# Kernel tuning notes

Hardware: AMD Instinct MI355X
Metric: run time of the kernel (lower is better)

## Reference

```python
import jax, jax.numpy as jnp
import numpy as np

N, E, G, H = 4096, 8192, 64, 128  # nodes, edges, graphs, hidden dim
NODE_DIM, EDGE_DIM = 11, 5


def _linear_params(key, fan_in, fan_out):
    kw, kb = jax.random.split(key)
    s = 1.0 / np.sqrt(fan_in)
    w = jax.random.uniform(kw, (fan_in, fan_out), minval=-s, maxval=s, dtype=jnp.float32)
    b = jax.random.uniform(kb, (fan_out,), minval=-s, maxval=s, dtype=jnp.float32)
    return w, b


def setup_inputs() -> dict:
    key = jax.random.key(0)
    ks = jax.random.split(key, 10)
    x = jax.random.normal(ks[0], (N, NODE_DIM), dtype=jnp.float32)
    edge_attr = jax.random.normal(ks[1], (E, EDGE_DIM), dtype=jnp.float32)
    edge_index = jax.random.randint(ks[2], (2, E), 0, N, dtype=jnp.int64)
    batch = jnp.sort(jax.random.randint(ks[3], (N,), 0, G, dtype=jnp.int64))
    # preprocess MLP: node_dim -> 128 -> 128
    p1_w, p1_b = _linear_params(ks[4], NODE_DIM, H)
    p2_w, p2_b = _linear_params(ks[5], H, H)
    # edge net: edge_dim -> 128 -> 256 -> 128 -> 128*128 (ReLU between, none after last)
    e1_w, e1_b = _linear_params(ks[6], EDGE_DIM, 128)
    e2_w, e2_b = _linear_params(ks[7], 128, 256)
    e3_w, e3_b = _linear_params(ks[8], 256, 128)
    e4_w, e4_b = _linear_params(ks[9], 128, H * H)
    return {"x": x, "edge_attr": edge_attr, "edge_index": edge_index, "batch": batch,
            "p1_w": p1_w, "p1_b": p1_b, "p2_w": p2_w, "p2_b": p2_b,
            "e1_w": e1_w, "e1_b": e1_b, "e2_w": e2_w, "e2_b": e2_b,
            "e3_w": e3_w, "e3_b": e3_b, "e4_w": e4_w, "e4_b": e4_b}


def reference(x, edge_attr, edge_index, batch,
              p1_w, p1_b, p2_w, p2_b,
              e1_w, e1_b, e2_w, e2_b, e3_w, e3_b, e4_w, e4_b):
    # node preprocess MLP (maps 11-dim features to 128 so NNConv dims are consistent)
    h = jax.nn.relu(x @ p1_w + p1_b) @ p2_w + p2_b  # [N, H]
    # edge network -> per-edge weight matrix [E, H, H]
    e = jax.nn.relu(edge_attr @ e1_w + e1_b)
    e = jax.nn.relu(e @ e2_w + e2_b)
    e = jax.nn.relu(e @ e3_w + e3_b)
    W = (e @ e4_w + e4_b).reshape(E, H, H)
    # NNConv (root_weight=False, bias=False, aggr='mean'):
    src, dst = edge_index[0], edge_index[1]
    msg = jnp.einsum('ei,eio->eo', h[src], W)  # gather + per-edge matmul, [E, H]
    agg = jax.ops.segment_sum(msg, dst, num_segments=N)
    cnt = jax.ops.segment_sum(jnp.ones((E,), msg.dtype), dst, num_segments=N)
    h_out = agg / jnp.maximum(cnt, 1.0)[:, None]  # scatter-mean, [N, H]
    # global add pool over graphs
    pooled = jax.ops.segment_sum(h_out, batch, num_segments=G)  # [G, H]
    return pooled
```

## Files before the change

### kernel.cpp

```cpp
#include <hip/hip_runtime.h>
#include <stdint.h>
#include <stddef.h>

typedef unsigned short ushort_t;
typedef __attribute__((ext_vector_type(8))) short short8;
typedef __attribute__((ext_vector_type(4))) short short4v;
typedef __attribute__((ext_vector_type(4))) float f32x4;
typedef __attribute__((ext_vector_type(4))) unsigned int uint4v;

#define GL2LDS(gsrc, ldst) \
  __builtin_amdgcn_global_load_lds((const __attribute__((address_space(1))) void*)(gsrc), \
                                   (__attribute__((address_space(3))) void*)(ldst), 16, 0, 0)

__device__ __forceinline__ float bf2f(ushort_t u) {
  union { unsigned int i; float f; } v; v.i = ((unsigned int)u) << 16; return v.f;
}
__device__ __forceinline__ ushort_t f2bf(float f) {
  unsigned int u = __builtin_bit_cast(unsigned int, f);
  unsigned int r = (u + 0x7fffu + ((u >> 16) & 1u)) >> 16;
  return (ushort_t)r;
}

__global__ void k_prep(const float* __restrict__ e4w, const float* __restrict__ e4b,
                       ushort_t* __restrict__ e4wT) {
  __shared__ float t[128][65];
  int c0 = blockIdx.x * 64;
  int tid = threadIdx.x;
  for (int it = 0; it < 32; ++it) {
    int idx = it * 256 + tid;
    int cc = idx >> 7, oo = idx & 127;
    int c = c0 + cc;
    float v = (c < 16384) ? e4w[(size_t)c * 128 + oo] : e4b[(size_t)(c - 16384) * 128 + oo];
    t[oo][cc] = v;
  }
  __syncthreads();
  for (int it = 0; it < 32; ++it) {
    int idx = it * 256 + tid;
    int oo = idx >> 6, cc = idx & 63;
    e4wT[(size_t)oo * 16512 + c0 + cc] = f2bf(t[oo][cc]);
  }
}

__global__ void k_node(const float* __restrict__ x, const float* __restrict__ p1w,
                       const float* __restrict__ p1b, const float* __restrict__ p2w,
                       const float* __restrict__ p2b, ushort_t* __restrict__ h_node) {
  __shared__ float xs[8][12];
  __shared__ float t1[8][128];
  int n0 = blockIdx.x * 8, tid = threadIdx.x;
  if (tid < 88) { int n = tid / 11, j = tid % 11; xs[n][j] = x[(size_t)(n0 + n) * 11 + j]; }
  __syncthreads();
  for (int it = 0; it < 4; ++it) {
    int p = it * 256 + tid;
    int n = p >> 7, o = p & 127;
    float a = p1b[o];
#pragma unroll
    for (int j = 0; j < 11; ++j) a += xs[n][j] * p1w[j * 128 + o];
    t1[n][o] = fmaxf(a, 0.f);
  }
  __syncthreads();
  {
    int o = tid & 127, nb = tid >> 7;
    float a0 = p2b[o], a1_ = a0, a2_ = a0, a3_ = a0;
    for (int k4 = 0; k4 < 32; ++k4) {
      float w0 = p2w[(k4 * 4 + 0) * 128 + o];
      float w1 = p2w[(k4 * 4 + 1) * 128 + o];
      float w2 = p2w[(k4 * 4 + 2) * 128 + o];
      float w3 = p2w[(k4 * 4 + 3) * 128 + o];
      float4 v0 = *(const float4*)&t1[nb + 0][k4 * 4];
      float4 v1 = *(const float4*)&t1[nb + 2][k4 * 4];
      float4 v2 = *(const float4*)&t1[nb + 4][k4 * 4];
      float4 v3 = *(const float4*)&t1[nb + 6][k4 * 4];
      a0 += v0.x * w0 + v0.y * w1 + v0.z * w2 + v0.w * w3;
      a1_ += v1.x * w0 + v1.y * w1 + v1.z * w2 + v1.w * w3;
      a2_ += v2.x * w0 + v2.y * w1 + v2.z * w2 + v2.w * w3;
      a3_ += v3.x * w0 + v3.y * w1 + v3.z * w2 + v3.w * w3;
    }
    h_node[(size_t)(n0 + nb + 0) * 128 + o] = f2bf(a0);
    h_node[(size_t)(n0 + nb + 2) * 128 + o] = f2bf(a1_);
    h_node[(size_t)(n0 + nb + 4) * 128 + o] = f2bf(a2_);
    h_node[(size_t)(n0 + nb + 6) * 128 + o] = f2bf(a3_);
  }
}

__global__ void k_edge(const float* __restrict__ ea, const int* __restrict__ eidx,
                       const ushort_t* __restrict__ h_node,
                       const float* __restrict__ e1w, const float* __restrict__ e1b,
                       const float* __restrict__ e2w, const float* __restrict__ e2b,
                       const float* __restrict__ e3w, const float* __restrict__ e3b,
                       ushort_t* __restrict__ e3T, ushort_t* __restrict__ h_src) {
  __shared__ float eas[16][6];
  __shared__ float a1[16][128];
  __shared__ float a2[16][256];
  __shared__ float a3[16][129];
  __shared__ int srcs[16];
  int e0 = blockIdx.x * 16, tid = threadIdx.x;
  if (tid < 80) { int n = tid / 5, j = tid % 5; eas[n][j] = ea[(size_t)(e0 + n) * 5 + j]; }
  if (tid < 16) srcs[tid] = eidx[e0 + tid];
  __syncthreads();
  for (int it = 0; it < 8; ++it) {
    int p = it * 256 + tid;
    int n = p >> 7, o = p & 127;
    h_src[(size_t)(e0 + n) * 128 + o] = h_node[(size_t)srcs[n] * 128 + o];
  }
  for (int it = 0; it < 8; ++it) {
    int p = it * 256 + tid;
    int n = p >> 7, o = p & 127;
    float a = e1b[o];
#pragma unroll
    for (int j = 0; j < 5; ++j) a += eas[n][j] * e1w[j * 128 + o];
    a1[n][o] = fmaxf(a, 0.f);
  }
  __syncthreads();
  {
    int o = tid;
    float acc[16];
#pragma unroll
    for (int n = 0; n < 16; ++n) acc[n] = e2b[o];
    for (int k4 = 0; k4 < 32; ++k4) {
      float w0 = e2w[(k4 * 4 + 0) * 256 + o];
      float w1 = e2w[(k4 * 4 + 1) * 256 + o];
      float w2 = e2w[(k4 * 4 + 2) * 256 + o];
      float w3 = e2w[(k4 * 4 + 3) * 256 + o];
#pragma unroll
      for (int n = 0; n < 16; ++n) {
        float4 av = *(const float4*)&a1[n][k4 * 4];
        acc[n] += av.x * w0 + av.y * w1 + av.z * w2 + av.w * w3;
      }
    }
#pragma unroll
    for (int n = 0; n < 16; ++n) a2[n][o] = fmaxf(acc[n], 0.f);
  }
  __syncthreads();
  {
    int o = tid & 127, nh = tid >> 7;
    float acc[8];
#pragma unroll
    for (int n = 0; n < 8; ++n) acc[n] = e3b[o];
    for (int k4 = 0; k4 < 64; ++k4) {
      float w0 = e3w[(k4 * 4 + 0) * 128 + o];
      float w1 = e3w[(k4 * 4 + 1) * 128 + o];
      float w2 = e3w[(k4 * 4 + 2) * 128 + o];
      float w3 = e3w[(k4 * 4 + 3) * 128 + o];
#pragma unroll
      for (int n = 0; n < 8; ++n) {
        float4 av = *(const float4*)&a2[nh * 8 + n][k4 * 4];
        acc[n] += av.x * w0 + av.y * w1 + av.z * w2 + av.w * w3;
      }
    }
#pragma unroll
    for (int n = 0; n < 8; ++n) a3[nh * 8 + n][o] = fmaxf(acc[n], 0.f);
  }
  __syncthreads();
  {
    int o = tid;
    if (o < 128) {
      uint4v q0, q1;
      q0.x = (unsigned)f2bf(a3[0][o]) | ((unsigned)f2bf(a3[1][o]) << 16);
      q0.y = (unsigned)f2bf(a3[2][o]) | ((unsigned)f2bf(a3[3][o]) << 16);
      q0.z = (unsigned)f2bf(a3[4][o]) | ((unsigned)f2bf(a3[5][o]) << 16);
      q0.w = (unsigned)f2bf(a3[6][o]) | ((unsigned)f2bf(a3[7][o]) << 16);
      q1.x = (unsigned)f2bf(a3[8][o]) | ((unsigned)f2bf(a3[9][o]) << 16);
      q1.y = (unsigned)f2bf(a3[10][o]) | ((unsigned)f2bf(a3[11][o]) << 16);
      q1.z = (unsigned)f2bf(a3[12][o]) | ((unsigned)f2bf(a3[13][o]) << 16);
      q1.w = (unsigned)f2bf(a3[14][o]) | ((unsigned)f2bf(a3[15][o]) << 16);
      *(uint4v*)(e3T + (size_t)o * 8192 + e0) = q0;
      *(uint4v*)(e3T + (size_t)o * 8192 + e0 + 8) = q1;
    }
  }
}

__launch_bounds__(256, 2)
__global__ void k_gemm(const ushort_t* __restrict__ h_src, const ushort_t* __restrict__ e3T,
                       const ushort_t* __restrict__ e4wT, ushort_t* __restrict__ partial) {
  __shared__ ushort_t bufA[2][16384];
  __shared__ ushort_t e3s[2048];

  int tid = threadIdx.x;
  int w = tid >> 6, ln = tid & 63;
  int g = ln >> 4, l15 = ln & 15;
  int bid = blockIdx.x;
  int mt = bid >> 3, s = bid & 7;
  int e0 = mt * 128;
  int t0 = s * 16;
  int nt = (s == 7) ? 17 : 16;

  {
    const ushort_t* hbase = h_src + (size_t)e0 * 128;
    for (int it = 0; it < 8; ++it) {
      int chunk = it * 256 + tid;
      int r = chunk >> 4;
      int Gt = (chunk & 15) ^ (r & 15);
      GL2LDS(hbase + r * 128 + Gt * 8, (char*)&bufA[0][0] + (it * 256 + w * 64) * 16);
    }
    {
      int chunk = tid;
      int tl = chunk >> 4;
      int cc = (chunk & 15) * 8;
      GL2LDS(e3T + (size_t)(t0 + tl) * 8192 + e0 + cc, (char*)&e3s[0] + (w * 64) * 16);
    }
  }
  asm volatile("s_waitcnt vmcnt(0)" ::: "memory");
  __builtin_amdgcn_s_barrier();
  asm volatile("" ::: "memory");

  short8 afr[2][4];
#pragma unroll
  for (int rf = 0; rf < 2; ++rf)
#pragma unroll
    for (int ks = 0; ks < 4; ++ks) {
      int row = w * 32 + rf * 16 + l15;
      int gr = (ks * 4 + g) ^ (row & 15);
      afr[rf][ks] = *(const short8*)((const char*)&bufA[0][0] + row * 256 + gr * 16);
    }
  asm volatile("s_waitcnt lgkmcnt(0)" ::: "memory");
  __builtin_amdgcn_s_barrier();
  asm volatile("" ::: "memory");

  auto stageB = [&](int b, int tg) {
    const ushort_t* wbase = e4wT + (size_t)tg * 128;
    for (int it = 0; it < 8; ++it) {
      int chunk = it * 256 + tid;
      int r = chunk >> 4;
      int Gt = (chunk & 15) ^ (r & 15);
      GL2LDS(wbase + (size_t)r * 16512 + Gt * 8, (char*)&bufA[b][0] + (it * 256 + w * 64) * 16);
    }
  };
  stageB(0, t0);
  stageB(1, t0 + 1);

  float acc[2][8][4];
#pragma unroll
  for (int rf = 0; rf < 2; ++rf)
#pragma unroll
    for (int cf = 0; cf < 8; ++cf)
#pragma unroll
      for (int r2 = 0; r2 < 4; ++r2) acc[rf][cf][r2] = 0.f;

  const f32x4 zero4 = {0.f, 0.f, 0.f, 0.f};

  for (int tl = 0; tl < nt; ++tl) {
    if (tl + 1 < nt) { asm volatile("s_waitcnt vmcnt(8)" ::: "memory"); }
    else             { asm volatile("s_waitcnt vmcnt(0)" ::: "memory"); }
    __builtin_amdgcn_s_barrier();
    asm volatile("" ::: "memory");
    int cur = tl & 1;
    int tg = t0 + tl;

    float sc[2][4];
    if (tg < 128) {
#pragma unroll
      for (int rf = 0; rf < 2; ++rf) {
        int row = w * 32 + rf * 16 + g * 4;
        short4v ev = *(const short4v*)((const char*)&e3s[0] + tl * 256 + row * 2);
#pragma unroll
        for (int r2 = 0; r2 < 4; ++r2) sc[rf][r2] = bf2f((ushort_t)ev[r2]);
      }
    } else {
#pragma unroll
      for (int rf = 0; rf < 2; ++rf)
#pragma unroll
        for (int r2 = 0; r2 < 4; ++r2) sc[rf][r2] = 1.f;
    }

    f32x4 part[2][8];
#pragma unroll
    for (int ks = 0; ks < 4; ++ks) {
#pragma unroll
      for (int ch = 0; ch < 2; ++ch) {
        short8 bfr[4];
#pragma unroll
        for (int cc = 0; cc < 4; ++cc) {
          int cf = ch * 4 + cc;
          int nrow = cf * 16 + l15;
          int gr = (ks * 4 + g) ^ (nrow & 15);
          bfr[cc] = *(const short8*)((const char*)&bufA[cur][0] + nrow * 256 + gr * 16);
        }
#pragma unroll
        for (int rf = 0; rf < 2; ++rf)
#pragma unroll
          for (int cc = 0; cc < 4; ++cc) {
            int cf = ch * 4 + cc;
            if (ks == 0)
              part[rf][cf] = __builtin_amdgcn_mfma_f32_16x16x32_bf16(afr[rf][0], bfr[cc], zero4, 0, 0, 0);
            else
              part[rf][cf] = __builtin_amdgcn_mfma_f32_16x16x32_bf16(afr[rf][ks], bfr[cc], part[rf][cf], 0, 0, 0);
          }
      }
    }
#pragma unroll
    for (int rf = 0; rf < 2; ++rf)
#pragma unroll
      for (int cf = 0; cf < 8; ++cf)
#pragma unroll
        for (int r2 = 0; r2 < 4; ++r2) acc[rf][cf][r2] += sc[rf][r2] * part[rf][cf][r2];

    asm volatile("s_waitcnt lgkmcnt(0)" ::: "memory");
    __builtin_amdgcn_s_barrier();
    asm volatile("" ::: "memory");
    if (tl + 2 < nt) stageB(cur, t0 + tl + 2);
  }

#pragma unroll
  for (int rf = 0; rf < 2; ++rf)
#pragma unroll
    for (int cf = 0; cf < 8; ++cf)
#pragma unroll
      for (int r2 = 0; r2 < 4; ++r2) {
        int row = w * 32 + rf * 16 + g * 4 + r2;
        int col = cf * 16 + l15;
        partial[((size_t)s * 8192 + e0 + row) * 128 + col] = f2bf(acc[rf][cf][r2]);
      }
}

__global__ void k_reduce(const ushort_t* __restrict__ partial, const int* __restrict__ eidx,
                         float* __restrict__ agg, float* __restrict__ cnt) {
  int id = blockIdx.x * 256 + threadIdx.x;
  int e = id >> 7, o = id & 127;
  float v = 0.f;
#pragma unroll
  for (int s2 = 0; s2 < 8; ++s2) v += bf2f(partial[((size_t)s2 * 8192 + e) * 128 + o]);
  int d = eidx[8192 + e];
  atomicAdd(&agg[(size_t)d * 128 + o], v);
  if (o == 0) atomicAdd(&cnt[d], 1.0f);
}

__device__ __forceinline__ int lbound(const int* a, int n, int v) {
  int lo = 0, hi = n;
  while (lo < hi) { int m = (lo + hi) >> 1; if (a[m] < v) lo = m + 1; else hi = m; }
  return lo;
}

__global__ void k_pool(const float* __restrict__ agg, const float* __restrict__ cnt,
                       const int* __restrict__ batch, float* __restrict__ out) {
  int gph = blockIdx.x, o = threadIdx.x;
  int lo = lbound(batch, 4096, gph);
  int hi = lbound(batch, 4096, gph + 1);
  float a = 0.f;
  for (int n = lo; n < hi; ++n) a += agg[(size_t)n * 128 + o] / fmaxf(cnt[n], 1.0f);
  out[(size_t)gph * 128 + o] = a;
}

extern "C" void kernel_launch(void* const* d_in, const int* in_sizes, int n_in,
                              void* d_out, int out_size, void* d_ws, size_t ws_size,
                              hipStream_t stream) {
  (void)in_sizes; (void)n_in; (void)out_size; (void)ws_size;
  const float* x   = (const float*)d_in[0];
  const float* ea  = (const float*)d_in[1];
  const int*   ei  = (const int*)d_in[2];
  const int*   bat = (const int*)d_in[3];
  const float* p1w = (const float*)d_in[4];  const float* p1b = (const float*)d_in[5];
  const float* p2w = (const float*)d_in[6];  const float* p2b = (const float*)d_in[7];
  const float* e1w = (const float*)d_in[8];  const float* e1b = (const float*)d_in[9];
  const float* e2w = (const float*)d_in[10]; const float* e2b = (const float*)d_in[11];
  const float* e3w = (const float*)d_in[12]; const float* e3b = (const float*)d_in[13];
  const float* e4w = (const float*)d_in[14]; const float* e4b = (const float*)d_in[15];

  char* ws = (char*)d_ws;
  ushort_t* e4wT   = (ushort_t*)(ws + 0);
  ushort_t* h_node = (ushort_t*)(ws + 4227072);
  ushort_t* h_srcp = (ushort_t*)(ws + 5275648);
  ushort_t* e3T    = (ushort_t*)(ws + 7372800);
  ushort_t* part   = (ushort_t*)(ws + 9469952);
  float*    agg    = (float*)(ws + 26247168);
  float*    cnt    = (float*)(ws + 28344320);

  hipMemsetAsync(ws + 26247168, 0, 2097152 + 16384, stream);

  k_prep  <<<258,  256, 0, stream>>>(e4w, e4b, e4wT);
  k_node  <<<512,  256, 0, stream>>>(x, p1w, p1b, p2w, p2b, h_node);
  k_edge  <<<512,  256, 0, stream>>>(ea, ei, h_node, e1w, e1b, e2w, e2b, e3w, e3b, e3T, h_srcp);
  k_gemm  <<<512,  256, 0, stream>>>(h_srcp, e3T, e4wT, part);
  k_reduce<<<4096, 256, 0, stream>>>(part, ei, agg, cnt);
  k_pool  <<<64,   128, 0, stream>>>(agg, cnt, bat, (float*)d_out);
}
```

Measured before the change: 205.0 us.

## Run edge MLP layers on bf16x3 MFMA and vectorize the reduce kernel

Replaces the scalar FP32 edge-network kernel with an MFMA-based version. It uses split-bf16 (hi/lo, three products) to keep near-FP32 accuracy for the 128->256 and 256->128 layers, and each block now handles 32 edges with 512 threads. Two new prep kernels split and transpose e2w/e3w into hi/lo bf16 on every call. The reduce kernel is also vectorized to read 8 bf16 values per thread and issue per-element atomics. This adds extra launches and some precision risk from the split approximation.

```diff
diff --git a/kernel.cpp b/kernel.cpp
--- a/kernel.cpp
+++ b/kernel.cpp
@@ -39,6 +39,19 @@
     int oo = idx >> 6, cc = idx & 63;
     e4wT[(size_t)oo * 16512 + c0 + cc] = f2bf(t[oo][cc]);
   }
+}
+
+__global__ void k_split_t(const float* __restrict__ in, ushort_t* __restrict__ oh,
+                          ushort_t* __restrict__ ol, int K, int lg2n) {
+  int id = blockIdx.x * 256 + threadIdx.x;
+  int N = 1 << lg2n;
+  if (id >= K * N) return;
+  int k = id >> lg2n, o = id & (N - 1);
+  float v = in[id];
+  ushort_t hb = f2bf(v);
+  float lo = v - bf2f(hb);
+  oh[(size_t)o * K + k] = hb;
+  ol[(size_t)o * K + k] = f2bf(lo);
 }
 
 __global__ void k_node(const float* __restrict__ x, const float* __restrict__ p1w,
@@ -82,90 +95,159 @@
   }
 }
 
-__global__ void k_edge(const float* __restrict__ ea, const int* __restrict__ eidx,
-                       const ushort_t* __restrict__ h_node,
-                       const float* __restrict__ e1w, const float* __restrict__ e1b,
-                       const float* __restrict__ e2w, const float* __restrict__ e2b,
-                       const float* __restrict__ e3w, const float* __restrict__ e3b,
-                       ushort_t* __restrict__ e3T, ushort_t* __restrict__ h_src) {
-  __shared__ float eas[16][6];
-  __shared__ float a1[16][128];
-  __shared__ float a2[16][256];
-  __shared__ float a3[16][129];
-  __shared__ int srcs[16];
-  int e0 = blockIdx.x * 16, tid = threadIdx.x;
-  if (tid < 80) { int n = tid / 5, j = tid % 5; eas[n][j] = ea[(size_t)(e0 + n) * 5 + j]; }
-  if (tid < 16) srcs[tid] = eidx[e0 + tid];
-  __syncthreads();
-  for (int it = 0; it < 8; ++it) {
-    int p = it * 256 + tid;
-    int n = p >> 7, o = p & 127;
-    h_src[(size_t)(e0 + n) * 128 + o] = h_node[(size_t)srcs[n] * 128 + o];
-  }
-  for (int it = 0; it < 8; ++it) {
-    int p = it * 256 + tid;
-    int n = p >> 7, o = p & 127;
-    float a = e1b[o];
-#pragma unroll
-    for (int j = 0; j < 5; ++j) a += eas[n][j] * e1w[j * 128 + o];
-    a1[n][o] = fmaxf(a, 0.f);
-  }
-  __syncthreads();
-  {
-    int o = tid;
-    float acc[16];
-#pragma unroll
-    for (int n = 0; n < 16; ++n) acc[n] = e2b[o];
-    for (int k4 = 0; k4 < 32; ++k4) {
-      float w0 = e2w[(k4 * 4 + 0) * 256 + o];
-      float w1 = e2w[(k4 * 4 + 1) * 256 + o];
-      float w2 = e2w[(k4 * 4 + 2) * 256 + o];
-      float w3 = e2w[(k4 * 4 + 3) * 256 + o];
-#pragma unroll
-      for (int n = 0; n < 16; ++n) {
-        float4 av = *(const float4*)&a1[n][k4 * 4];
-        acc[n] += av.x * w0 + av.y * w1 + av.z * w2 + av.w * w3;
-      }
-    }
-#pragma unroll
-    for (int n = 0; n < 16; ++n) a2[n][o] = fmaxf(acc[n], 0.f);
-  }
-  __syncthreads();
-  {
-    int o = tid & 127, nh = tid >> 7;
-    float acc[8];
-#pragma unroll
-    for (int n = 0; n < 8; ++n) acc[n] = e3b[o];
-    for (int k4 = 0; k4 < 64; ++k4) {
-      float w0 = e3w[(k4 * 4 + 0) * 128 + o];
-      float w1 = e3w[(k4 * 4 + 1) * 128 + o];
-      float w2 = e3w[(k4 * 4 + 2) * 128 + o];
-      float w3 = e3w[(k4 * 4 + 3) * 128 + o];
-#pragma unroll
-      for (int n = 0; n < 8; ++n) {
-        float4 av = *(const float4*)&a2[nh * 8 + n][k4 * 4];
-        acc[n] += av.x * w0 + av.y * w1 + av.z * w2 + av.w * w3;
-      }
-    }
-#pragma unroll
-    for (int n = 0; n < 8; ++n) a3[nh * 8 + n][o] = fmaxf(acc[n], 0.f);
-  }
-  __syncthreads();
-  {
-    int o = tid;
-    if (o < 128) {
-      uint4v q0, q1;
-      q0.x = (unsigned)f2bf(a3[0][o]) | ((unsigned)f2bf(a3[1][o]) << 16);
-      q0.y = (unsigned)f2bf(a3[2][o]) | ((unsigned)f2bf(a3[3][o]) << 16);
-      q0.z = (unsigned)f2bf(a3[4][o]) | ((unsigned)f2bf(a3[5][o]) << 16);
-      q0.w = (unsigned)f2bf(a3[6][o]) | ((unsigned)f2bf(a3[7][o]) << 16);
-      q1.x = (unsigned)f2bf(a3[8][o]) | ((unsigned)f2bf(a3[9][o]) << 16);
-      q1.y = (unsigned)f2bf(a3[10][o]) | ((unsigned)f2bf(a3[11][o]) << 16);
-      q1.z = (unsigned)f2bf(a3[12][o]) | ((unsigned)f2bf(a3[13][o]) << 16);
-      q1.w = (unsigned)f2bf(a3[14][o]) | ((unsigned)f2bf(a3[15][o]) << 16);
-      *(uint4v*)(e3T + (size_t)o * 8192 + e0) = q0;
-      *(uint4v*)(e3T + (size_t)o * 8192 + e0 + 8) = q1;
-    }
+__global__ void k_mlp(const float* __restrict__ ea, const int* __restrict__ eidx,
+                      const ushort_t* __restrict__ h_node,
+                      const float* __restrict__ e1w, const float* __restrict__ e1b,
+                      const ushort_t* __restrict__ w2h, const ushort_t* __restrict__ w2l,
+                      const float* __restrict__ e2b,
+                      const ushort_t* __restrict__ w3h, const ushort_t* __restrict__ w3l,
+                      const float* __restrict__ e3b,
+                      ushort_t* __restrict__ e3T, ushort_t* __restrict__ h_src) {
+  __shared__ float eas[32][6];
+  __shared__ int srcs[32];
+  __shared__ ushort_t a1h[32 * 136], a1l[32 * 136];
+  __shared__ ushort_t a2h[32 * 264], a2l[32 * 264];
+  __shared__ ushort_t a3t[128 * 40];
+
+  int tid = threadIdx.x;
+  int w = tid >> 6, ln = tid & 63, g = ln >> 4, l15 = ln & 15;
+  int e0 = blockIdx.x * 32;
+
+  if (tid < 160) { int n = tid / 5, j = tid % 5; eas[n][j] = ea[(size_t)(e0 + n) * 5 + j]; }
+  if (tid < 32) srcs[tid] = eidx[e0 + tid];
+  __syncthreads();
+
+  {
+    int n = tid >> 4, oc = (tid & 15) * 8;
+    *(short8*)(h_src + (size_t)(e0 + n) * 128 + oc) =
+        *(const short8*)(h_node + (size_t)srcs[n] * 128 + oc);
+  }
+
+  {
+    int n = tid >> 4, ob = (tid & 15) * 8;
+    float acc1[8];
+    float4 ba = *(const float4*)(e1b + ob);
+    float4 bb = *(const float4*)(e1b + ob + 4);
+    acc1[0] = ba.x; acc1[1] = ba.y; acc1[2] = ba.z; acc1[3] = ba.w;
+    acc1[4] = bb.x; acc1[5] = bb.y; acc1[6] = bb.z; acc1[7] = bb.w;
+#pragma unroll
+    for (int j = 0; j < 5; ++j) {
+      float aj = eas[n][j];
+      float4 wa = *(const float4*)(e1w + j * 128 + ob);
+      float4 wb = *(const float4*)(e1w + j * 128 + ob + 4);
+      acc1[0] = fmaf(aj, wa.x, acc1[0]); acc1[1] = fmaf(aj, wa.y, acc1[1]);
+      acc1[2] = fmaf(aj, wa.z, acc1[2]); acc1[3] = fmaf(aj, wa.w, acc1[3]);
+      acc1[4] = fmaf(aj, wb.x, acc1[4]); acc1[5] = fmaf(aj, wb.y, acc1[5]);
+      acc1[6] = fmaf(aj, wb.z, acc1[6]); acc1[7] = fmaf(aj, wb.w, acc1[7]);
+    }
+    short8 ph, pl;
+#pragma unroll
+    for (int q = 0; q < 8; ++q) {
+      float v = fmaxf(acc1[q], 0.f);
+      ushort_t hb = f2bf(v);
+      ph[q] = (short)hb;
+      pl[q] = (short)f2bf(v - bf2f(hb));
+    }
+    int addr = n * 136 + ob;
+    *(short8*)(a1h + addr) = ph;
+    *(short8*)(a1l + addr) = pl;
+  }
+  __syncthreads();
+
+  {
+    int cbase = w * 32;
+    f32x4 acc2[2][2];
+#pragma unroll
+    for (int rf = 0; rf < 2; ++rf)
+#pragma unroll
+      for (int cf = 0; cf < 2; ++cf) acc2[rf][cf] = (f32x4){0.f, 0.f, 0.f, 0.f};
+    short8 ah[2][4], al[2][4];
+#pragma unroll
+    for (int rf = 0; rf < 2; ++rf)
+#pragma unroll
+      for (int ks = 0; ks < 4; ++ks) {
+        int row = rf * 16 + l15;
+        int addr = row * 136 + (ks * 4 + g) * 8;
+        ah[rf][ks] = *(const short8*)(a1h + addr);
+        al[rf][ks] = *(const short8*)(a1l + addr);
+      }
+#pragma unroll
+    for (int ks = 0; ks < 4; ++ks) {
+#pragma unroll
+      for (int cf = 0; cf < 2; ++cf) {
+        int nrow = cbase + cf * 16 + l15;
+        size_t boff = (size_t)nrow * 128 + (ks * 4 + g) * 8;
+        short8 bh = *(const short8*)(w2h + boff);
+        short8 bl = *(const short8*)(w2l + boff);
+#pragma unroll
+        for (int rf = 0; rf < 2; ++rf) {
+          acc2[rf][cf] = __builtin_amdgcn_mfma_f32_16x16x32_bf16(ah[rf][ks], bh, acc2[rf][cf], 0, 0, 0);
+          acc2[rf][cf] = __builtin_amdgcn_mfma_f32_16x16x32_bf16(al[rf][ks], bh, acc2[rf][cf], 0, 0, 0);
+          acc2[rf][cf] = __builtin_amdgcn_mfma_f32_16x16x32_bf16(ah[rf][ks], bl, acc2[rf][cf], 0, 0, 0);
+        }
+      }
+    }
+#pragma unroll
+    for (int rf = 0; rf < 2; ++rf)
+#pragma unroll
+      for (int cf = 0; cf < 2; ++cf) {
+        int col = cbase + cf * 16 + l15;
+        float b = e2b[col];
+#pragma unroll
+        for (int r2 = 0; r2 < 4; ++r2) {
+          int row = rf * 16 + g * 4 + r2;
+          float v = fmaxf(acc2[rf][cf][r2] + b, 0.f);
+          ushort_t hb = f2bf(v);
+          int addr = row * 264 + col;
+          a2h[addr] = hb;
+          a2l[addr] = f2bf(v - bf2f(hb));
+        }
+      }
+  }
+  __syncthreads();
+
+  {
+    f32x4 acc3[2];
+    acc3[0] = (f32x4){0.f, 0.f, 0.f, 0.f};
+    acc3[1] = (f32x4){0.f, 0.f, 0.f, 0.f};
+    int nrow = w * 16 + l15;
+#pragma unroll
+    for (int ks = 0; ks < 8; ++ks) {
+      short8 a2hf[2], a2lf[2];
+#pragma unroll
+      for (int rf = 0; rf < 2; ++rf) {
+        int row = rf * 16 + l15;
+        int addr = row * 264 + (ks * 4 + g) * 8;
+        a2hf[rf] = *(const short8*)(a2h + addr);
+        a2lf[rf] = *(const short8*)(a2l + addr);
+      }
+      size_t boff = (size_t)nrow * 256 + (ks * 4 + g) * 8;
+      short8 bh = *(const short8*)(w3h + boff);
+      short8 bl = *(const short8*)(w3l + boff);
+#pragma unroll
+      for (int rf = 0; rf < 2; ++rf) {
+        acc3[rf] = __builtin_amdgcn_mfma_f32_16x16x32_bf16(a2hf[rf], bh, acc3[rf], 0, 0, 0);
+        acc3[rf] = __builtin_amdgcn_mfma_f32_16x16x32_bf16(a2lf[rf], bh, acc3[rf], 0, 0, 0);
+        acc3[rf] = __builtin_amdgcn_mfma_f32_16x16x32_bf16(a2hf[rf], bl, acc3[rf], 0, 0, 0);
+      }
+    }
+    int col = w * 16 + l15;
+    float b = e3b[col];
+#pragma unroll
+    for (int rf = 0; rf < 2; ++rf)
+#pragma unroll
+      for (int r2 = 0; r2 < 4; ++r2) {
+        int row = rf * 16 + g * 4 + r2;
+        float v = fmaxf(acc3[rf][r2] + b, 0.f);
+        a3t[col * 40 + row] = f2bf(v);
+      }
+  }
+  __syncthreads();
+
+  {
+    int o = tid >> 2, eq = (tid & 3) * 8;
+    short8 q = *(const short8*)(a3t + o * 40 + eq);
+    *(short8*)(e3T + (size_t)o * 8192 + e0 + eq) = q;
   }
 }
 
@@ -315,13 +397,21 @@
 __global__ void k_reduce(const ushort_t* __restrict__ partial, const int* __restrict__ eidx,
                          float* __restrict__ agg, float* __restrict__ cnt) {
   int id = blockIdx.x * 256 + threadIdx.x;
-  int e = id >> 7, o = id & 127;
-  float v = 0.f;
-#pragma unroll
-  for (int s2 = 0; s2 < 8; ++s2) v += bf2f(partial[((size_t)s2 * 8192 + e) * 128 + o]);
+  int e = id >> 4, oc = (id & 15) * 8;
+  float v[8];
+#pragma unroll
+  for (int q = 0; q < 8; ++q) v[q] = 0.f;
+#pragma unroll
+  for (int s2 = 0; s2 < 8; ++s2) {
+    short8 p = *(const short8*)(partial + ((size_t)s2 * 8192 + e) * 128 + oc);
+#pragma unroll
+    for (int q = 0; q < 8; ++q) v[q] += bf2f((ushort_t)p[q]);
+  }
   int d = eidx[8192 + e];
-  atomicAdd(&agg[(size_t)d * 128 + o], v);
-  if (o == 0) atomicAdd(&cnt[d], 1.0f);
+  float* dst = agg + (size_t)d * 128 + oc;
+#pragma unroll
+  for (int q = 0; q < 8; ++q) atomicAdd(dst + q, v[q]);
+  if ((id & 15) == 0) atomicAdd(&cnt[d], 1.0f);
 }
 
 __device__ __forceinline__ int lbound(const int* a, int n, int v) {
@@ -363,13 +453,20 @@
   ushort_t* part   = (ushort_t*)(ws + 9469952);
   float*    agg    = (float*)(ws + 26247168);
   float*    cnt    = (float*)(ws + 28344320);
+  ushort_t* w2h    = (ushort_t*)(ws + 28360704);
+  ushort_t* w2l    = (ushort_t*)(ws + 28426240);
+  ushort_t* w3h    = (ushort_t*)(ws + 28491776);
+  ushort_t* w3l    = (ushort_t*)(ws + 28557312);
 
   hipMemsetAsync(ws + 26247168, 0, 2097152 + 16384, stream);
 
-  k_prep  <<<258,  256, 0, stream>>>(e4w, e4b, e4wT);
-  k_node  <<<512,  256, 0, stream>>>(x, p1w, p1b, p2w, p2b, h_node);
-  k_edge  <<<512,  256, 0, stream>>>(ea, ei, h_node, e1w, e1b, e2w, e2b, e3w, e3b, e3T, h_srcp);
-  k_gemm  <<<512,  256, 0, stream>>>(h_srcp, e3T, e4wT, part);
-  k_reduce<<<4096, 256, 0, stream>>>(part, ei, agg, cnt);
-  k_pool  <<<64,   128, 0, stream>>>(agg, cnt, bat, (float*)d_out);
-}
+  k_prep   <<<258,  256, 0, stream>>>(e4w, e4b, e4wT);
+  k_split_t<<<128,  256, 0, stream>>>(e2w, w2h, w2l, 128, 8);
+  k_split_t<<<128,  256, 0, stream>>>(e3w, w3h, w3l, 256, 7);
+  k_node   <<<512,  256, 0, stream>>>(x, p1w, p1b, p2w, p2b, h_node);
+  k_mlp    <<<256,  512, 0, stream>>>(ea, ei, h_node, e1w, e1b, w2h, w2l, e2b,
+                                      w3h, w3l, e3b, e3T, h_srcp);
+  k_gemm   <<<512,  256, 0, stream>>>(h_srcp, e3T, e4wT, part);
+  k_reduce <<<512,  256, 0, stream>>>(part, ei, agg, cnt);
+  k_pool   <<<64,   128, 0, stream>>>(agg, cnt, bat, (float*)d_out);
+}
```

Measured after the change: 216.8 us. 1.06x slower.
